# Kernel optimization log

Measured on AMD Instinct MI355X. Metric: run time of the kernel, lower is better.

## Reference

```python
import jax, jax.numpy as jnp
import numpy as np

N_VOCAB = 100      # periodic-table embedding size
N_GAUSS = 300      # SchNet-standard RBF expansion
RBF_CUTOFF = 30.0
RBF_GAMMA = 10.0
N_INTERACTIONS = 3
LOG2 = float(np.log(2.0))


def ssp(x):
    # shifted softplus: log(0.5*exp(x) + 0.5) = softplus(x) - log(2)
    return jax.nn.softplus(x) - LOG2


def setup_inputs() -> dict:
    key = jax.random.key(0)
    ks = jax.random.split(key, 16)
    B, N, F, NF = 32, 128, 128, 128
    s = lambda k, shape, sc=0.1: (jax.random.normal(k, shape, dtype=jnp.float32) * sc)
    return {
        "z": jax.random.randint(ks[0], (B, N), 0, N_VOCAB),
        "r": jax.random.normal(ks[1], (B, N, 3), dtype=jnp.float32) * 3.0,
        "emb": s(ks[2], (N_VOCAB, F)),
        "w_in2f": s(ks[3], (F, NF)),
        "w_f1": s(ks[4], (N_GAUSS, NF)), "b_f1": jnp.zeros((NF,), jnp.float32),
        "w_f2": s(ks[5], (NF, NF)),      "b_f2": jnp.zeros((NF,), jnp.float32),
        "w_f2out": s(ks[6], (NF, F)),    "b_f2out": jnp.zeros((F,), jnp.float32),
        "w_out": s(ks[7], (F, F)),       "b_out": jnp.zeros((F,), jnp.float32),
        "w_aw1": s(ks[8], (F, F)),       "b_aw1": jnp.zeros((F,), jnp.float32),
        "w_aw2": s(ks[9], (F, 1)),       "b_aw2": jnp.zeros((1,), jnp.float32),
    }


def reference(z, r, emb, w_in2f, w_f1, b_f1, w_f2, b_f2,
              w_f2out, b_f2out, w_out, b_out, w_aw1, b_aw1, w_aw2, b_aw2):
    # ---- pairwise distances + RBF expansion (shared across interactions) ----
    diff = r[:, :, None, :] - r[:, None, :, :]            # [B,N,N,3]
    d = jnp.sqrt(jnp.sum(diff * diff, axis=-1) + 1e-12)    # [B,N,N]
    centers = jnp.linspace(0.0, RBF_CUTOFF, N_GAUSS, dtype=jnp.float32)
    rbf = jnp.exp(-RBF_GAMMA * (d[..., None] - centers) ** 2)  # [B,N,N,G]
    # filter network (distance-only -> hoisted out of the interaction loop;
    # the single InteractionLayer is weight-shared across all passes)
    W = ssp(jnp.einsum('bijg,gf->bijf', rbf, w_f1) + b_f1)
    W = jnp.einsum('bijf,fh->bijh', W, w_f2) + b_f2         # [B,N,N,NF]

    # ---- atom embedding ----
    x = emb[z]                                              # [B,N,F]

    # ---- interaction blocks (shared weights, applied n_interactions times) ----
    for _ in range(N_INTERACTIONS):
        f = jnp.einsum('bnf,fh->bnh', x, w_in2f)            # atom-wise, no bias
        y = jnp.einsum('bijh,bjh->bih', W, f)               # cfconv aggregation
        y = ssp(jnp.einsum('bnh,hf->bnf', y, w_f2out) + b_f2out)
        v = jnp.einsum('bnf,fg->bng', y, w_out) + b_out
        x = x + v                                           # residual update

    # ---- atom-wise readout ----
    x = ssp(jnp.einsum('bnf,fg->bng', x, w_aw1) + b_aw1)
    out = jnp.einsum('bnf,fo->bno', x, w_aw2) + b_aw2       # [B,N,1]
    return out
```

## Files before the change

### kernel.cpp

```cpp
#include <hip/hip_runtime.h>
#include <hip/hip_bf16.h>
#include <stdint.h>

typedef __bf16 bf16x8 __attribute__((ext_vector_type(8)));
typedef float  f32x4  __attribute__((ext_vector_type(4)));
typedef unsigned short u16;
typedef unsigned int   u32;
typedef u16 u16x4 __attribute__((ext_vector_type(4)));
typedef u32 u32x4 __attribute__((ext_vector_type(4)));

#define B_  32
#define N_  128
#define F_  128
#define G_  300
#define GP  320
#define TAB_N 4096
#define TAB_SCALE 128.0f

__device__ __forceinline__ u16 f2b(float f){
  union { float f; u32 u; } x; x.f = f;
  u32 r = x.u + 0x7FFFu + ((x.u >> 16) & 1u);
  return (u16)(r >> 16);
}
__device__ __forceinline__ u32 pack2bf(float a, float b){
  return __builtin_amdgcn_perm(__float_as_uint(b) + 0x8000u,
                               __float_as_uint(a) + 0x8000u, 0x07060302u);
}
__device__ __forceinline__ float sspf(float x){
  return fmaxf(x, 0.0f) + __logf(0.5f + 0.5f*__expf(-fabsf(x)));
}
__device__ __forceinline__ f32x4 mfma16(bf16x8 a, bf16x8 b, f32x4 c){
  return __builtin_amdgcn_mfma_f32_16x16x32_bf16(a, b, c, 0, 0, 0);
}

__global__ __launch_bounds__(256) void k_setup(const float* __restrict__ w_f1,
                                               const float* __restrict__ w_f2,
                                               const float* __restrict__ w_in2f,
                                               const float* __restrict__ w_f2out,
                                               const float* __restrict__ w_out,
                                               const float* __restrict__ w_aw1,
                                               u16* __restrict__ w1t,
                                               u16* __restrict__ w2t,
                                               u16* __restrict__ wi2t,
                                               u16* __restrict__ w2outT,
                                               u16* __restrict__ woutT,
                                               u16* __restrict__ waw1T){
  int idx = blockIdx.x*256 + threadIdx.x;
  if (idx < 128*GP){
    int h = idx / GP, g = idx % GP;
    w1t[idx] = (g < G_) ? f2b(w_f1[g*F_ + h]) : (u16)0;
  } else {
    int j = idx - 128*GP;
    int which = j >> 14;
    int rr = j & 16383;
    int h = rr >> 7, k = rr & 127;
    const float* src; u16* dst;
    switch (which){
      case 0:  src = w_f2;    dst = w2t;    break;
      case 1:  src = w_in2f;  dst = wi2t;   break;
      case 2:  src = w_f2out; dst = w2outT; break;
      case 3:  src = w_out;   dst = woutT;  break;
      default: src = w_aw1;   dst = waw1T;  break;
    }
    dst[h*128 + k] = f2b(src[k*128 + h]);
  }
}

__global__ __launch_bounds__(256) void k_gentab(const u16* __restrict__ w1t,
                                                const u16* __restrict__ w2t,
                                                const float* __restrict__ b_f1,
                                                const float* __restrict__ b_f2,
                                                u16* __restrict__ tab){
  __shared__ __attribute__((aligned(16))) u16 w1s[16][136];
  int tid = threadIdx.x, lane = tid & 63, wave = tid >> 6;
  int m = lane & 15, q = lane >> 4;
  int t0 = blockIdx.x * 16;
  int C0 = wave*32;
  const float K2 = 14.4269504089f;
  const float DC = 30.0f/299.0f;
  float d = (float)(t0 + m) * (1.0f/TAB_SCALE);

  f32x4 acc[2];
  acc[0] = (f32x4){0.f,0.f,0.f,0.f}; acc[1] = (f32x4){0.f,0.f,0.f,0.f};
  #pragma unroll
  for (int ks = 0; ks < 10; ++ks){
    int kb = ks*32 + q*8;
    u32x4 au;
    #pragma unroll
    for (int t2 = 0; t2 < 4; ++t2){
      int k0 = kb + t2*2;
      float u0 = d - DC*(float)k0;
      float u1 = d - DC*(float)(k0 + 1);
      float e0 = __builtin_amdgcn_exp2f(-K2*u0*u0);
      float e1 = __builtin_amdgcn_exp2f(-K2*u1*u1);
      au[t2] = pack2bf(e0, e1);
    }
    bf16x8 af = __builtin_bit_cast(bf16x8, au);
    #pragma unroll
    for (int ni = 0; ni < 2; ++ni){
      bf16x8 bfv = *reinterpret_cast<const bf16x8*>(w1t + (size_t)(C0 + ni*16 + m)*GP + kb);
      acc[ni] = mfma16(af, bfv, acc[ni]);
    }
  }
  #pragma unroll
  for (int ni = 0; ni < 2; ++ni)
    #pragma unroll
    for (int rr = 0; rr < 4; ++rr){
      int col = C0 + ni*16 + m;
      w1s[q*4 + rr][col & 127] = f2b(sspf(acc[ni][rr] + b_f1[col]));
    }
  __syncthreads();

  f32x4 acc2[2];
  acc2[0] = (f32x4){0.f,0.f,0.f,0.f}; acc2[1] = (f32x4){0.f,0.f,0.f,0.f};
  #pragma unroll
  for (int ks = 0; ks < 4; ++ks){
    int kb = ks*32 + q*8;
    bf16x8 af = *reinterpret_cast<const bf16x8*>(&w1s[m][kb]);
    #pragma unroll
    for (int ni = 0; ni < 2; ++ni){
      bf16x8 bfv = *reinterpret_cast<const bf16x8*>(w2t + (size_t)(C0 + ni*16 + m)*128 + kb);
      acc2[ni] = mfma16(af, bfv, acc2[ni]);
    }
  }
  #pragma unroll
  for (int ni = 0; ni < 2; ++ni)
    #pragma unroll
    for (int rr = 0; rr < 4; ++rr){
      int col = C0 + ni*16 + m;
      tab[(size_t)(t0 + q*4 + rr)*F_ + col] = f2b(acc2[ni][rr] + b_f2[col]);
    }
}

__global__ __launch_bounds__(256) void k_lin(const int* __restrict__ z,
                                             const float* __restrict__ emb,
                                             const u16* __restrict__ wi2t,
                                             u16* __restrict__ fb){
  int bi = blockIdx.x;
  int b = bi >> 2, qd = bi & 3;
  int tid = threadIdx.x, lane = tid & 63, wave = tid >> 6;
  int m = lane & 15, q = lane >> 4;
  int R0 = qd*32 + (wave >> 1)*16;
  int C0 = (wave & 1)*64;
  int row = R0 + m;
  const float* erow = emb + (size_t)z[b*N_ + row]*F_;
  f32x4 acc[4];
  #pragma unroll
  for (int ni = 0; ni < 4; ++ni) acc[ni] = (f32x4){0.f,0.f,0.f,0.f};
  #pragma unroll
  for (int ks = 0; ks < 4; ++ks){
    int k0 = ks*32 + q*8;
    float4 e0 = *reinterpret_cast<const float4*>(erow + k0);
    float4 e1 = *reinterpret_cast<const float4*>(erow + k0 + 4);
    u32x4 au;
    au[0] = pack2bf(e0.x, e0.y); au[1] = pack2bf(e0.z, e0.w);
    au[2] = pack2bf(e1.x, e1.y); au[3] = pack2bf(e1.z, e1.w);
    bf16x8 af = __builtin_bit_cast(bf16x8, au);
    #pragma unroll
    for (int ni = 0; ni < 4; ++ni){
      bf16x8 bfv = *reinterpret_cast<const bf16x8*>(wi2t + (size_t)(C0 + ni*16 + m)*F_ + k0);
      acc[ni] = mfma16(af, bfv, acc[ni]);
    }
  }
  u16* fbb = fb + (size_t)b*N_*F_;
  #pragma unroll
  for (int ni = 0; ni < 4; ++ni)
    #pragma unroll
    for (int rr = 0; rr < 4; ++rr)
      fbb[(size_t)(R0 + q*4 + rr)*F_ + C0 + ni*16 + m] = f2b(acc[ni][rr]);
}

__global__ __launch_bounds__(256, 4) void k_conv(const u16* __restrict__ fb,
                                                 const u16* __restrict__ tab,
                                                 const float* __restrict__ r,
                                                 float* __restrict__ y){
  __shared__ float rsh[128][3];
  __shared__ u16   dIdxS[512];
  __shared__ float dFracS[512];
  __shared__ __attribute__((aligned(16))) float psh[4][4*132];

  int bid = blockIdx.x;
  int b = bid >> 5, i0 = (bid & 31)*4;
  int tid = threadIdx.x;

  if (tid < 128){
    const float* rp = r + (size_t)(b*N_ + tid)*3;
    rsh[tid][0] = rp[0]; rsh[tid][1] = rp[1]; rsh[tid][2] = rp[2];
  }
  __syncthreads();

  #pragma unroll
  for (int t = 0; t < 2; ++t){
    int p = tid + t*256;
    int il = p >> 7, j = p & 127;
    int ia = i0 + il;
    float dx = rsh[ia][0] - rsh[j][0];
    float dy = rsh[ia][1] - rsh[j][1];
    float dz = rsh[ia][2] - rsh[j][2];
    float d = sqrtf(fmaf(dx,dx, fmaf(dy,dy, fmaf(dz,dz, 1e-12f))));
    float u = fminf(d * TAB_SCALE, (float)(TAB_N - 1));
    int ix = (int)u; if (ix > TAB_N - 2) ix = TAB_N - 2;
    dIdxS[p]  = (u16)ix;
    dFracS[p] = u - (float)ix;
  }
  __syncthreads();

  int chg = tid & 15, il = (tid >> 4) & 3, jq = tid >> 6;
  int h0 = chg*8;
  float yv[8] = {0,0,0,0,0,0,0,0};
  const u16* tb0 = tab + h0;
  const u16* fbp = fb + (size_t)b*N_*F_ + h0;
  int pbase = il*128 + jq*32;
  #pragma unroll 4
  for (int jj = 0; jj < 32; ++jj){
    int p = pbase + jj;
    u32 ix  = dIdxS[p];
    float fr = dFracS[p];
    const u16* rp = tb0 + ((size_t)ix << 7);
    bf16x8 ta  = *reinterpret_cast<const bf16x8*>(rp);
    bf16x8 tb2 = *reinterpret_cast<const bf16x8*>(rp + F_);
    bf16x8 fv  = *reinterpret_cast<const bf16x8*>(fbp + (size_t)(jq*32 + jj)*F_);
    #pragma unroll
    for (int t = 0; t < 8; ++t){
      float a = (float)ta[t];
      float w = fmaf(fr, (float)tb2[t] - a, a);
      yv[t] = fmaf(w, (float)fv[t], yv[t]);
    }
  }
  {
    float* pp = &psh[jq][il*132 + h0];
    *reinterpret_cast<float4*>(pp)     = (float4){yv[0], yv[1], yv[2], yv[3]};
    *reinterpret_cast<float4*>(pp + 4) = (float4){yv[4], yv[5], yv[6], yv[7]};
  }
  __syncthreads();
  #pragma unroll
  for (int t = 0; t < 2; ++t){
    int o = tid + t*256;
    int oil = o >> 7, ch = o & 127;
    int ofs = oil*132 + ch;
    y[((size_t)(b*N_ + i0 + oil))*F_ + ch] =
      psh[0][ofs] + psh[1][ofs] + psh[2][ofs] + psh[3][ofs];
  }
}

__global__ __launch_bounds__(256) void k_mlp(const float* __restrict__ y,
                                             float* __restrict__ x,
                                             const int* __restrict__ z,
                                             const float* __restrict__ emb,
                                             const u16* __restrict__ w2outT,
                                             const float* __restrict__ b_f2out,
                                             const u16* __restrict__ woutT,
                                             const float* __restrict__ b_out,
                                             const u16* __restrict__ wi2t,
                                             const u16* __restrict__ waw1T,
                                             const float* __restrict__ b_aw1,
                                             const float* __restrict__ w_aw2,
                                             const float* __restrict__ b_aw2,
                                             u16* __restrict__ fb,
                                             float* __restrict__ outp,
                                             int first, int mode){
  __shared__ __attribute__((aligned(16))) u16 ab[16][136];
  __shared__ float cs[16][132];
  __shared__ float psum[16][8];
  __shared__ int zsh[16];
  int tid = threadIdx.x, lane = tid & 63, wave = tid >> 6;
  int m = lane & 15, q = lane >> 4;
  int bid = blockIdx.x;
  int b = bid >> 3, R0 = (bid & 7)*16;
  int C0 = wave*32;

  if (first && tid < 16) zsh[tid] = z[b*N_ + R0 + tid];
  {
    int row = tid >> 4, c8 = (tid & 15)*8;
    const float* yp = y + ((size_t)(b*N_ + R0 + row))*F_ + c8;
    float4 a = *reinterpret_cast<const float4*>(yp);
    float4 bq = *reinterpret_cast<const float4*>(yp + 4);
    u32x4 au;
    au[0] = pack2bf(a.x, a.y);  au[1] = pack2bf(a.z, a.w);
    au[2] = pack2bf(bq.x, bq.y); au[3] = pack2bf(bq.z, bq.w);
    *reinterpret_cast<u32x4*>(&ab[row][c8]) = au;
  }
  __syncthreads();

  f32x4 acc[2];
  acc[0] = (f32x4){0.f,0.f,0.f,0.f}; acc[1] = (f32x4){0.f,0.f,0.f,0.f};
  #pragma unroll
  for (int ks = 0; ks < 4; ++ks){
    int kb = ks*32 + q*8;
    bf16x8 af = *reinterpret_cast<const bf16x8*>(&ab[m][kb]);
    #pragma unroll
    for (int ni = 0; ni < 2; ++ni){
      bf16x8 bfv = *reinterpret_cast<const bf16x8*>(w2outT + (size_t)(C0 + ni*16 + m)*F_ + kb);
      acc[ni] = mfma16(af, bfv, acc[ni]);
    }
  }
  __syncthreads();
  #pragma unroll
  for (int ni = 0; ni < 2; ++ni)
    #pragma unroll
    for (int rr = 0; rr < 4; ++rr){
      int col = C0 + ni*16 + m;
      ab[q*4 + rr][col & 127] = f2b(sspf(acc[ni][rr] + b_f2out[col]));
    }
  __syncthreads();

  f32x4 acc2[2];
  acc2[0] = (f32x4){0.f,0.f,0.f,0.f}; acc2[1] = (f32x4){0.f,0.f,0.f,0.f};
  #pragma unroll
  for (int ks = 0; ks < 4; ++ks){
    int kb = ks*32 + q*8;
    bf16x8 af = *reinterpret_cast<const bf16x8*>(&ab[m][kb]);
    #pragma unroll
    for (int ni = 0; ni < 2; ++ni){
      bf16x8 bfv = *reinterpret_cast<const bf16x8*>(woutT + (size_t)(C0 + ni*16 + m)*F_ + kb);
      acc2[ni] = mfma16(af, bfv, acc2[ni]);
    }
  }
  __syncthreads();
  #pragma unroll
  for (int ni = 0; ni < 2; ++ni)
    #pragma unroll
    for (int rr = 0; rr < 4; ++rr){
      int row = q*4 + rr, col = C0 + ni*16 + m;
      size_t xo = (size_t)(b*N_ + R0 + row)*F_ + col;
      float xi = first ? emb[(size_t)zsh[row]*F_ + col] : x[xo];
      float nv = xi + acc2[ni][rr] + b_out[col];
      if (mode == 0) x[xo] = nv;
      ab[row][col & 127] = f2b(nv);
    }
  __syncthreads();

  const u16* w3 = (mode == 0) ? wi2t : waw1T;
  f32x4 acc3[2];
  acc3[0] = (f32x4){0.f,0.f,0.f,0.f}; acc3[1] = (f32x4){0.f,0.f,0.f,0.f};
  #pragma unroll
  for (int ks = 0; ks < 4; ++ks){
    int kb = ks*32 + q*8;
    bf16x8 af = *reinterpret_cast<const bf16x8*>(&ab[m][kb]);
    #pragma unroll
    for (int ni = 0; ni < 2; ++ni){
      bf16x8 bfv = *reinterpret_cast<const bf16x8*>(w3 + (size_t)(C0 + ni*16 + m)*F_ + kb);
      acc3[ni] = mfma16(af, bfv, acc3[ni]);
    }
  }
  if (mode == 0){
    #pragma unroll
    for (int ni = 0; ni < 2; ++ni)
      #pragma unroll
      for (int rr = 0; rr < 4; ++rr)
        fb[(size_t)(b*N_ + R0 + q*4 + rr)*F_ + C0 + ni*16 + m] = f2b(acc3[ni][rr]);
  } else {
    #pragma unroll
    for (int ni = 0; ni < 2; ++ni)
      #pragma unroll
      for (int rr = 0; rr < 4; ++rr){
        int col = C0 + ni*16 + m;
        cs[q*4 + rr][col] = sspf(acc3[ni][rr] + b_aw1[col]) * w_aw2[col];
      }
    __syncthreads();
    if (tid < 128){
      int row = tid >> 3, seg = tid & 7;
      float s = 0.f;
      #pragma unroll
      for (int t = 0; t < 16; ++t) s += cs[row][seg*16 + t];
      psum[row][seg] = s;
    }
    __syncthreads();
    if (tid < 16){
      float s = 0.f;
      #pragma unroll
      for (int t = 0; t < 8; ++t) s += psum[tid][t];
      outp[b*N_ + R0 + tid] = s + b_aw2[0];
    }
  }
}

extern "C" void kernel_launch(void* const* d_in, const int* in_sizes, int n_in,
                              void* d_out, int out_size, void* d_ws, size_t ws_size,
                              hipStream_t stream){
  const int*   z       = (const int*)d_in[0];
  const float* r       = (const float*)d_in[1];
  const float* emb     = (const float*)d_in[2];
  const float* w_in2f  = (const float*)d_in[3];
  const float* w_f1    = (const float*)d_in[4];
  const float* b_f1    = (const float*)d_in[5];
  const float* w_f2    = (const float*)d_in[6];
  const float* b_f2    = (const float*)d_in[7];
  const float* w_f2out = (const float*)d_in[8];
  const float* b_f2out = (const float*)d_in[9];
  const float* w_out   = (const float*)d_in[10];
  const float* b_out   = (const float*)d_in[11];
  const float* w_aw1   = (const float*)d_in[12];
  const float* b_aw1   = (const float*)d_in[13];
  const float* w_aw2   = (const float*)d_in[14];
  const float* b_aw2   = (const float*)d_in[15];

  char* ws = (char*)d_ws;
  float* x     = (float*)(ws);
  float* y     = (float*)(ws + 2097152);
  u16*   fbuf  = (u16*)(ws + 4194304);
  u16*   tab   = (u16*)(ws + 5242880);
  u16*   w1t   = (u16*)(ws + 6291456);
  u16*   w2t   = (u16*)(ws + 6373376);
  u16*   wi2t  = (u16*)(ws + 6406144);
  u16*   w2oT  = (u16*)(ws + 6438912);
  u16*   woT   = (u16*)(ws + 6471680);
  u16*   waw1T = (u16*)(ws + 6504448);

  k_setup<<<480, 256, 0, stream>>>(w_f1, w_f2, w_in2f, w_f2out, w_out, w_aw1,
                                   w1t, w2t, wi2t, w2oT, woT, waw1T);
  k_gentab<<<256, 256, 0, stream>>>(w1t, w2t, b_f1, b_f2, tab);
  k_lin<<<128, 256, 0, stream>>>(z, emb, wi2t, fbuf);
  k_conv<<<1024, 256, 0, stream>>>(fbuf, tab, r, y);
  k_mlp<<<256, 256, 0, stream>>>(y, x, z, emb, w2oT, b_f2out, woT, b_out,
                                 wi2t, waw1T, b_aw1, w_aw2, b_aw2,
                                 fbuf, (float*)d_out, 1, 0);
  k_conv<<<1024, 256, 0, stream>>>(fbuf, tab, r, y);
  k_mlp<<<256, 256, 0, stream>>>(y, x, z, emb, w2oT, b_f2out, woT, b_out,
                                 wi2t, waw1T, b_aw1, w_aw2, b_aw2,
                                 fbuf, (float*)d_out, 0, 0);
  k_conv<<<1024, 256, 0, stream>>>(fbuf, tab, r, y);
  k_mlp<<<256, 256, 0, stream>>>(y, x, z, emb, w2oT, b_f2out, woT, b_out,
                                 wi2t, waw1T, b_aw1, w_aw2, b_aw2,
                                 fbuf, (float*)d_out, 0, 1);
}
```

Baseline: 167.9 us.

## Precompute distance indices, drop interpolation with finer table, stage features in LDS

The gentab, lin and distance-index computations are merged into one prep kernel, so the pairwise distance indices are computed once rather than in every interaction pass. The filter table resolution is doubled, which allows nearest-neighbour lookup in place of linear interpolation and halves the table reads per pair. The conv kernel now splits channels across two blocks, stages the per-molecule feature slice in LDS, and writes y as bf16, which shrinks traffic into the MLP. Nearest-lookup quantisation and bf16 y add some accuracy risk, and the larger table increases cache footprint.

```diff
diff --git a/kernel.cpp b/kernel.cpp
--- a/kernel.cpp
+++ b/kernel.cpp
@@ -3,6 +3,7 @@
 #include <stdint.h>
 
 typedef __bf16 bf16x8 __attribute__((ext_vector_type(8)));
+typedef __bf16 bf16x4 __attribute__((ext_vector_type(4)));
 typedef float  f32x4  __attribute__((ext_vector_type(4)));
 typedef unsigned short u16;
 typedef unsigned int   u32;
@@ -14,8 +15,8 @@
 #define F_  128
 #define G_  300
 #define GP  320
-#define TAB_N 4096
-#define TAB_SCALE 128.0f
+#define TAB_N 8192
+#define TAB_SCALE 256.0f
 
 __device__ __forceinline__ u16 f2b(float f){
   union { float f; u32 u; } x; x.f = f;
@@ -66,184 +67,194 @@
   }
 }
 
-__global__ __launch_bounds__(256) void k_gentab(const u16* __restrict__ w1t,
-                                                const u16* __restrict__ w2t,
-                                                const float* __restrict__ b_f1,
-                                                const float* __restrict__ b_f2,
-                                                u16* __restrict__ tab){
+__global__ __launch_bounds__(256) void k_prep(const u16* __restrict__ w1t,
+                                              const u16* __restrict__ w2t,
+                                              const float* __restrict__ b_f1,
+                                              const float* __restrict__ b_f2,
+                                              u16* __restrict__ tab,
+                                              const int* __restrict__ z,
+                                              const float* __restrict__ emb,
+                                              const u16* __restrict__ wi2t,
+                                              u16* __restrict__ fb,
+                                              const float* __restrict__ r,
+                                              u16* __restrict__ dIdx){
   __shared__ __attribute__((aligned(16))) u16 w1s[16][136];
+  __shared__ float rshp[128][3];
+  int blk = blockIdx.x;
   int tid = threadIdx.x, lane = tid & 63, wave = tid >> 6;
   int m = lane & 15, q = lane >> 4;
-  int t0 = blockIdx.x * 16;
-  int C0 = wave*32;
-  const float K2 = 14.4269504089f;
-  const float DC = 30.0f/299.0f;
-  float d = (float)(t0 + m) * (1.0f/TAB_SCALE);
-
-  f32x4 acc[2];
-  acc[0] = (f32x4){0.f,0.f,0.f,0.f}; acc[1] = (f32x4){0.f,0.f,0.f,0.f};
-  #pragma unroll
-  for (int ks = 0; ks < 10; ++ks){
-    int kb = ks*32 + q*8;
-    u32x4 au;
-    #pragma unroll
-    for (int t2 = 0; t2 < 4; ++t2){
-      int k0 = kb + t2*2;
-      float u0 = d - DC*(float)k0;
-      float u1 = d - DC*(float)(k0 + 1);
-      float e0 = __builtin_amdgcn_exp2f(-K2*u0*u0);
-      float e1 = __builtin_amdgcn_exp2f(-K2*u1*u1);
-      au[t2] = pack2bf(e0, e1);
-    }
-    bf16x8 af = __builtin_bit_cast(bf16x8, au);
-    #pragma unroll
-    for (int ni = 0; ni < 2; ++ni){
-      bf16x8 bfv = *reinterpret_cast<const bf16x8*>(w1t + (size_t)(C0 + ni*16 + m)*GP + kb);
-      acc[ni] = mfma16(af, bfv, acc[ni]);
-    }
-  }
-  #pragma unroll
-  for (int ni = 0; ni < 2; ++ni)
-    #pragma unroll
-    for (int rr = 0; rr < 4; ++rr){
-      int col = C0 + ni*16 + m;
-      w1s[q*4 + rr][col & 127] = f2b(sspf(acc[ni][rr] + b_f1[col]));
-    }
-  __syncthreads();
-
-  f32x4 acc2[2];
-  acc2[0] = (f32x4){0.f,0.f,0.f,0.f}; acc2[1] = (f32x4){0.f,0.f,0.f,0.f};
-  #pragma unroll
-  for (int ks = 0; ks < 4; ++ks){
-    int kb = ks*32 + q*8;
-    bf16x8 af = *reinterpret_cast<const bf16x8*>(&w1s[m][kb]);
-    #pragma unroll
-    for (int ni = 0; ni < 2; ++ni){
-      bf16x8 bfv = *reinterpret_cast<const bf16x8*>(w2t + (size_t)(C0 + ni*16 + m)*128 + kb);
-      acc2[ni] = mfma16(af, bfv, acc2[ni]);
-    }
-  }
-  #pragma unroll
-  for (int ni = 0; ni < 2; ++ni)
-    #pragma unroll
-    for (int rr = 0; rr < 4; ++rr){
-      int col = C0 + ni*16 + m;
-      tab[(size_t)(t0 + q*4 + rr)*F_ + col] = f2b(acc2[ni][rr] + b_f2[col]);
-    }
-}
-
-__global__ __launch_bounds__(256) void k_lin(const int* __restrict__ z,
-                                             const float* __restrict__ emb,
-                                             const u16* __restrict__ wi2t,
-                                             u16* __restrict__ fb){
-  int bi = blockIdx.x;
-  int b = bi >> 2, qd = bi & 3;
-  int tid = threadIdx.x, lane = tid & 63, wave = tid >> 6;
-  int m = lane & 15, q = lane >> 4;
-  int R0 = qd*32 + (wave >> 1)*16;
-  int C0 = (wave & 1)*64;
-  int row = R0 + m;
-  const float* erow = emb + (size_t)z[b*N_ + row]*F_;
-  f32x4 acc[4];
-  #pragma unroll
-  for (int ni = 0; ni < 4; ++ni) acc[ni] = (f32x4){0.f,0.f,0.f,0.f};
-  #pragma unroll
-  for (int ks = 0; ks < 4; ++ks){
-    int k0 = ks*32 + q*8;
-    float4 e0 = *reinterpret_cast<const float4*>(erow + k0);
-    float4 e1 = *reinterpret_cast<const float4*>(erow + k0 + 4);
-    u32x4 au;
-    au[0] = pack2bf(e0.x, e0.y); au[1] = pack2bf(e0.z, e0.w);
-    au[2] = pack2bf(e1.x, e1.y); au[3] = pack2bf(e1.z, e1.w);
-    bf16x8 af = __builtin_bit_cast(bf16x8, au);
-    #pragma unroll
-    for (int ni = 0; ni < 4; ++ni){
-      bf16x8 bfv = *reinterpret_cast<const bf16x8*>(wi2t + (size_t)(C0 + ni*16 + m)*F_ + k0);
-      acc[ni] = mfma16(af, bfv, acc[ni]);
-    }
-  }
-  u16* fbb = fb + (size_t)b*N_*F_;
-  #pragma unroll
-  for (int ni = 0; ni < 4; ++ni)
-    #pragma unroll
-    for (int rr = 0; rr < 4; ++rr)
-      fbb[(size_t)(R0 + q*4 + rr)*F_ + C0 + ni*16 + m] = f2b(acc[ni][rr]);
-}
-
-__global__ __launch_bounds__(256, 4) void k_conv(const u16* __restrict__ fb,
+
+  if (blk < 512){
+    int t0 = blk * 16;
+    int C0 = wave*32;
+    const float K2 = 14.4269504089f;
+    const float DC = 30.0f/299.0f;
+    float d = (float)(t0 + m) * (1.0f/TAB_SCALE);
+    f32x4 acc[2];
+    acc[0] = (f32x4){0.f,0.f,0.f,0.f}; acc[1] = (f32x4){0.f,0.f,0.f,0.f};
+    #pragma unroll
+    for (int ks = 0; ks < 10; ++ks){
+      int kb = ks*32 + q*8;
+      u32x4 au;
+      #pragma unroll
+      for (int t2 = 0; t2 < 4; ++t2){
+        int k0 = kb + t2*2;
+        float u0 = d - DC*(float)k0;
+        float u1 = d - DC*(float)(k0 + 1);
+        float e0 = __builtin_amdgcn_exp2f(-K2*u0*u0);
+        float e1 = __builtin_amdgcn_exp2f(-K2*u1*u1);
+        au[t2] = pack2bf(e0, e1);
+      }
+      bf16x8 af = __builtin_bit_cast(bf16x8, au);
+      #pragma unroll
+      for (int ni = 0; ni < 2; ++ni){
+        bf16x8 bfv = *reinterpret_cast<const bf16x8*>(w1t + (size_t)(C0 + ni*16 + m)*GP + kb);
+        acc[ni] = mfma16(af, bfv, acc[ni]);
+      }
+    }
+    #pragma unroll
+    for (int ni = 0; ni < 2; ++ni)
+      #pragma unroll
+      for (int rr = 0; rr < 4; ++rr){
+        int col = C0 + ni*16 + m;
+        w1s[q*4 + rr][col & 127] = f2b(sspf(acc[ni][rr] + b_f1[col]));
+      }
+    __syncthreads();
+    f32x4 acc2[2];
+    acc2[0] = (f32x4){0.f,0.f,0.f,0.f}; acc2[1] = (f32x4){0.f,0.f,0.f,0.f};
+    #pragma unroll
+    for (int ks = 0; ks < 4; ++ks){
+      int kb = ks*32 + q*8;
+      bf16x8 af = *reinterpret_cast<const bf16x8*>(&w1s[m][kb]);
+      #pragma unroll
+      for (int ni = 0; ni < 2; ++ni){
+        bf16x8 bfv = *reinterpret_cast<const bf16x8*>(w2t + (size_t)(C0 + ni*16 + m)*128 + kb);
+        acc2[ni] = mfma16(af, bfv, acc2[ni]);
+      }
+    }
+    #pragma unroll
+    for (int ni = 0; ni < 2; ++ni)
+      #pragma unroll
+      for (int rr = 0; rr < 4; ++rr){
+        int col = C0 + ni*16 + m;
+        tab[(size_t)(t0 + q*4 + rr)*F_ + col] = f2b(acc2[ni][rr] + b_f2[col]);
+      }
+  } else if (blk < 640){
+    int bi = blk - 512;
+    int b = bi >> 2, qd = bi & 3;
+    int R0 = qd*32 + (wave >> 1)*16;
+    int C0 = (wave & 1)*64;
+    int row = R0 + m;
+    const float* erow = emb + (size_t)z[b*N_ + row]*F_;
+    f32x4 acc[4];
+    #pragma unroll
+    for (int ni = 0; ni < 4; ++ni) acc[ni] = (f32x4){0.f,0.f,0.f,0.f};
+    #pragma unroll
+    for (int ks = 0; ks < 4; ++ks){
+      int k0 = ks*32 + q*8;
+      float4 e0 = *reinterpret_cast<const float4*>(erow + k0);
+      float4 e1 = *reinterpret_cast<const float4*>(erow + k0 + 4);
+      u32x4 au;
+      au[0] = pack2bf(e0.x, e0.y); au[1] = pack2bf(e0.z, e0.w);
+      au[2] = pack2bf(e1.x, e1.y); au[3] = pack2bf(e1.z, e1.w);
+      bf16x8 af = __builtin_bit_cast(bf16x8, au);
+      #pragma unroll
+      for (int ni = 0; ni < 4; ++ni){
+        bf16x8 bfv = *reinterpret_cast<const bf16x8*>(wi2t + (size_t)(C0 + ni*16 + m)*F_ + k0);
+        acc[ni] = mfma16(af, bfv, acc[ni]);
+      }
+    }
+    u16* fbb = fb + (size_t)b*N_*F_;
+    #pragma unroll
+    for (int ni = 0; ni < 4; ++ni)
+      #pragma unroll
+      for (int rr = 0; rr < 4; ++rr)
+        fbb[(size_t)(R0 + q*4 + rr)*F_ + C0 + ni*16 + m] = f2b(acc[ni][rr]);
+  } else {
+    int pb = blk - 640;
+    int b = pb >> 1, i0p = (pb & 1)*64;
+    if (tid < 128){
+      const float* rp = r + (size_t)(b*N_ + tid)*3;
+      rshp[tid][0] = rp[0]; rshp[tid][1] = rp[1]; rshp[tid][2] = rp[2];
+    }
+    __syncthreads();
+    #pragma unroll
+    for (int t = 0; t < 32; ++t){
+      int p = t*256 + tid;
+      int il = p >> 7, j = p & 127;
+      int i = i0p + il;
+      float dx = rshp[i][0] - rshp[j][0];
+      float dy = rshp[i][1] - rshp[j][1];
+      float dz = rshp[i][2] - rshp[j][2];
+      float d = sqrtf(fmaf(dx,dx, fmaf(dy,dy, fmaf(dz,dz, 1e-12f))));
+      int ix = (int)(d * TAB_SCALE + 0.5f);
+      if (ix > TAB_N - 1) ix = TAB_N - 1;
+      dIdx[((size_t)(b*N_ + i))*N_ + j] = (u16)ix;
+    }
+  }
+}
+
+__global__ __launch_bounds__(256, 6) void k_conv(const u16* __restrict__ fb,
                                                  const u16* __restrict__ tab,
-                                                 const float* __restrict__ r,
-                                                 float* __restrict__ y){
-  __shared__ float rsh[128][3];
-  __shared__ u16   dIdxS[512];
-  __shared__ float dFracS[512];
-  __shared__ __attribute__((aligned(16))) float psh[4][4*132];
-
+                                                 const u16* __restrict__ dIdx,
+                                                 u16* __restrict__ yb){
+  __shared__ __attribute__((aligned(16))) u16 fsl[128][68];
+  __shared__ u16 dIdxS[4*132];
   int bid = blockIdx.x;
-  int b = bid >> 5, i0 = (bid & 31)*4;
+  int b = bid >> 6, it = (bid >> 1) & 31, chh = bid & 1;
+  int i0 = it*4, c0 = chh*64;
   int tid = threadIdx.x;
-
-  if (tid < 128){
-    const float* rp = r + (size_t)(b*N_ + tid)*3;
-    rsh[tid][0] = rp[0]; rsh[tid][1] = rp[1]; rsh[tid][2] = rp[2];
-  }
-  __syncthreads();
-
-  #pragma unroll
-  for (int t = 0; t < 2; ++t){
-    int p = tid + t*256;
+  {
+    int row = tid >> 1, half = (tid & 1)*32;
+    const u16x4* s4 = reinterpret_cast<const u16x4*>(fb + ((size_t)(b*N_ + row))*F_ + c0 + half);
+    #pragma unroll
+    for (int k = 0; k < 8; ++k)
+      *reinterpret_cast<u16x4*>(&fsl[row][half + k*4]) = s4[k];
+  }
+  {
+    u32 v = *reinterpret_cast<const u32*>(dIdx + ((size_t)(b*N_ + i0))*N_ + 2*tid);
+    int p = 2*tid;
     int il = p >> 7, j = p & 127;
-    int ia = i0 + il;
-    float dx = rsh[ia][0] - rsh[j][0];
-    float dy = rsh[ia][1] - rsh[j][1];
-    float dz = rsh[ia][2] - rsh[j][2];
-    float d = sqrtf(fmaf(dx,dx, fmaf(dy,dy, fmaf(dz,dz, 1e-12f))));
-    float u = fminf(d * TAB_SCALE, (float)(TAB_N - 1));
-    int ix = (int)u; if (ix > TAB_N - 2) ix = TAB_N - 2;
-    dIdxS[p]  = (u16)ix;
-    dFracS[p] = u - (float)ix;
-  }
-  __syncthreads();
-
-  int chg = tid & 15, il = (tid >> 4) & 3, jq = tid >> 6;
+    *reinterpret_cast<u32*>(&dIdxS[il*132 + j]) = v;
+  }
+  __syncthreads();
+
+  int jq = tid >> 5, il = (tid >> 3) & 3, chg = tid & 7;
   int h0 = chg*8;
+  const u16* tb0 = tab + c0 + h0;
   float yv[8] = {0,0,0,0,0,0,0,0};
-  const u16* tb0 = tab + h0;
-  const u16* fbp = fb + (size_t)b*N_*F_ + h0;
-  int pbase = il*128 + jq*32;
-  #pragma unroll 4
-  for (int jj = 0; jj < 32; ++jj){
-    int p = pbase + jj;
-    u32 ix  = dIdxS[p];
-    float fr = dFracS[p];
-    const u16* rp = tb0 + ((size_t)ix << 7);
-    bf16x8 ta  = *reinterpret_cast<const bf16x8*>(rp);
-    bf16x8 tb2 = *reinterpret_cast<const bf16x8*>(rp + F_);
-    bf16x8 fv  = *reinterpret_cast<const bf16x8*>(fbp + (size_t)(jq*32 + jj)*F_);
-    #pragma unroll
-    for (int t = 0; t < 8; ++t){
-      float a = (float)ta[t];
-      float w = fmaf(fr, (float)tb2[t] - a, a);
-      yv[t] = fmaf(w, (float)fv[t], yv[t]);
-    }
-  }
+  #pragma unroll
+  for (int jj = 0; jj < 16; ++jj){
+    int j = jq*16 + jj;
+    u32 ix = dIdxS[il*132 + j];
+    bf16x8 ta = *reinterpret_cast<const bf16x8*>(tb0 + (size_t)ix*F_);
+    bf16x4 fa = *reinterpret_cast<const bf16x4*>(&fsl[j][h0]);
+    bf16x4 fc = *reinterpret_cast<const bf16x4*>(&fsl[j][h0 + 4]);
+    yv[0] = fmaf((float)ta[0], (float)fa[0], yv[0]);
+    yv[1] = fmaf((float)ta[1], (float)fa[1], yv[1]);
+    yv[2] = fmaf((float)ta[2], (float)fa[2], yv[2]);
+    yv[3] = fmaf((float)ta[3], (float)fa[3], yv[3]);
+    yv[4] = fmaf((float)ta[4], (float)fc[0], yv[4]);
+    yv[5] = fmaf((float)ta[5], (float)fc[1], yv[5]);
+    yv[6] = fmaf((float)ta[6], (float)fc[2], yv[6]);
+    yv[7] = fmaf((float)ta[7], (float)fc[3], yv[7]);
+  }
+  __syncthreads();
+  float* pshf = reinterpret_cast<float*>(&fsl[0][0]);
   {
-    float* pp = &psh[jq][il*132 + h0];
+    float* pp = pshf + (jq*4 + il)*64 + h0;
     *reinterpret_cast<float4*>(pp)     = (float4){yv[0], yv[1], yv[2], yv[3]};
     *reinterpret_cast<float4*>(pp + 4) = (float4){yv[4], yv[5], yv[6], yv[7]};
   }
   __syncthreads();
-  #pragma unroll
-  for (int t = 0; t < 2; ++t){
-    int o = tid + t*256;
-    int oil = o >> 7, ch = o & 127;
-    int ofs = oil*132 + ch;
-    y[((size_t)(b*N_ + i0 + oil))*F_ + ch] =
-      psh[0][ofs] + psh[1][ofs] + psh[2][ofs] + psh[3][ofs];
-  }
-}
-
-__global__ __launch_bounds__(256) void k_mlp(const float* __restrict__ y,
+  int ilo = tid >> 6, cho = tid & 63;
+  float s = 0.f;
+  #pragma unroll
+  for (int t = 0; t < 8; ++t) s += pshf[(t*4 + ilo)*64 + cho];
+  yb[((size_t)(b*N_ + i0 + ilo))*F_ + c0 + cho] = f2b(s);
+}
+
+__global__ __launch_bounds__(256) void k_mlp(const u16* __restrict__ yb,
                                              float* __restrict__ x,
                                              const int* __restrict__ z,
                                              const float* __restrict__ emb,
@@ -272,13 +283,8 @@
   if (first && tid < 16) zsh[tid] = z[b*N_ + R0 + tid];
   {
     int row = tid >> 4, c8 = (tid & 15)*8;
-    const float* yp = y + ((size_t)(b*N_ + R0 + row))*F_ + c8;
-    float4 a = *reinterpret_cast<const float4*>(yp);
-    float4 bq = *reinterpret_cast<const float4*>(yp + 4);
-    u32x4 au;
-    au[0] = pack2bf(a.x, a.y);  au[1] = pack2bf(a.z, a.w);
-    au[2] = pack2bf(bq.x, bq.y); au[3] = pack2bf(bq.z, bq.w);
-    *reinterpret_cast<u32x4*>(&ab[row][c8]) = au;
+    *reinterpret_cast<bf16x8*>(&ab[row][c8]) =
+      *reinterpret_cast<const bf16x8*>(yb + ((size_t)(b*N_ + R0 + row))*F_ + c8);
   }
   __syncthreads();
 
@@ -397,30 +403,31 @@
 
   char* ws = (char*)d_ws;
   float* x     = (float*)(ws);
-  float* y     = (float*)(ws + 2097152);
-  u16*   fbuf  = (u16*)(ws + 4194304);
-  u16*   tab   = (u16*)(ws + 5242880);
-  u16*   w1t   = (u16*)(ws + 6291456);
-  u16*   w2t   = (u16*)(ws + 6373376);
-  u16*   wi2t  = (u16*)(ws + 6406144);
-  u16*   w2oT  = (u16*)(ws + 6438912);
-  u16*   woT   = (u16*)(ws + 6471680);
-  u16*   waw1T = (u16*)(ws + 6504448);
+  u16*   yb    = (u16*)(ws + 2097152);
+  u16*   fbuf  = (u16*)(ws + 3145728);
+  u16*   tab   = (u16*)(ws + 4194304);
+  u16*   dIdx  = (u16*)(ws + 6291456);
+  u16*   w1t   = (u16*)(ws + 7340032);
+  u16*   w2t   = (u16*)(ws + 7421952);
+  u16*   wi2t  = (u16*)(ws + 7454720);
+  u16*   w2oT  = (u16*)(ws + 7487488);
+  u16*   woT   = (u16*)(ws + 7520256);
+  u16*   waw1T = (u16*)(ws + 7553024);
 
   k_setup<<<480, 256, 0, stream>>>(w_f1, w_f2, w_in2f, w_f2out, w_out, w_aw1,
                                    w1t, w2t, wi2t, w2oT, woT, waw1T);
-  k_gentab<<<256, 256, 0, stream>>>(w1t, w2t, b_f1, b_f2, tab);
-  k_lin<<<128, 256, 0, stream>>>(z, emb, wi2t, fbuf);
-  k_conv<<<1024, 256, 0, stream>>>(fbuf, tab, r, y);
-  k_mlp<<<256, 256, 0, stream>>>(y, x, z, emb, w2oT, b_f2out, woT, b_out,
+  k_prep<<<704, 256, 0, stream>>>(w1t, w2t, b_f1, b_f2, tab,
+                                  z, emb, wi2t, fbuf, r, dIdx);
+  k_conv<<<2048, 256, 0, stream>>>(fbuf, tab, dIdx, yb);
+  k_mlp<<<256, 256, 0, stream>>>(yb, x, z, emb, w2oT, b_f2out, woT, b_out,
                                  wi2t, waw1T, b_aw1, w_aw2, b_aw2,
                                  fbuf, (float*)d_out, 1, 0);
-  k_conv<<<1024, 256, 0, stream>>>(fbuf, tab, r, y);
-  k_mlp<<<256, 256, 0, stream>>>(y, x, z, emb, w2oT, b_f2out, woT, b_out,
+  k_conv<<<2048, 256, 0, stream>>>(fbuf, tab, dIdx, yb);
+  k_mlp<<<256, 256, 0, stream>>>(yb, x, z, emb, w2oT, b_f2out, woT, b_out,
                                  wi2t, waw1T, b_aw1, w_aw2, b_aw2,
                                  fbuf, (float*)d_out, 0, 0);
-  k_conv<<<1024, 256, 0, stream>>>(fbuf, tab, r, y);
-  k_mlp<<<256, 256, 0, stream>>>(y, x, z, emb, w2oT, b_f2out, woT, b_out,
+  k_conv<<<2048, 256, 0, stream>>>(fbuf, tab, dIdx, yb);
+  k_mlp<<<256, 256, 0, stream>>>(yb, x, z, emb, w2oT, b_f2out, woT, b_out,
                                  wi2t, waw1T, b_aw1, w_aw2, b_aw2,
                                  fbuf, (float*)d_out, 0, 1);
 }
```

Measured after the change: 300.5 us. 79.0% more time.
